# Kernel tuning notes

Measured on AMD Instinct MI355X. Metric: run time of the kernel, lower is better.

The kernel has to match this reference:

```python
import jax, jax.numpy as jnp
import numpy as np

N_NODES = 50000
N_EDGES = 800000
IN_DIM = 128
HIDDEN = 256
N_CLASSES = 10
N_GRAPHS = 64


def setup_inputs() -> dict:
    key = jax.random.key(0)
    ks = jax.random.split(key, 12)
    x = jax.random.normal(ks[0], (N_NODES, IN_DIM), dtype=jnp.float32)
    edge_index = jax.random.randint(ks[1], (2, N_EDGES), 0, N_NODES, dtype=jnp.int64)
    batch = jnp.sort(jax.random.randint(ks[2], (N_NODES,), 0, N_GRAPHS, dtype=jnp.int64))
    s = 1.0 / np.sqrt(IN_DIM)
    sh = 1.0 / np.sqrt(HIDDEN)
    return {
        "x": x,
        "edge_index": edge_index,
        "batch": batch,
        # layer 0 (in_dim -> hidden), weights stored [in, out]
        "Wg0": jax.random.uniform(ks[3], (IN_DIM, HIDDEN), jnp.float32, -s, s),
        "Wl0": jax.random.uniform(ks[4], (IN_DIM, HIDDEN), jnp.float32, -s, s),
        "Ws0": jax.random.uniform(ks[5], (IN_DIM, HIDDEN), jnp.float32, -s, s),
        "b0": jnp.zeros((HIDDEN,), jnp.float32),
        # layer 1 (hidden -> hidden)
        "Wg1": jax.random.uniform(ks[6], (HIDDEN, HIDDEN), jnp.float32, -sh, sh),
        "Wl1": jax.random.uniform(ks[7], (HIDDEN, HIDDEN), jnp.float32, -sh, sh),
        "Ws1": jax.random.uniform(ks[8], (HIDDEN, HIDDEN), jnp.float32, -sh, sh),
        "b1": jnp.zeros((HIDDEN,), jnp.float32),
        # classifier (hidden -> num_classes)
        "Wc": jax.random.uniform(ks[9], (HIDDEN, N_CLASSES), jnp.float32, -sh, sh),
        "bc": jax.random.uniform(ks[10], (N_CLASSES,), jnp.float32, -sh, sh),
    }


def _demo_layer(h, src, dst, deg, Wg, Wl, Ws, b):
    # global transform on all nodes
    g = h @ Wg
    # per-node mean of neighbor features over outgoing edges (== degree-bucket mean)
    neigh_sum = jax.ops.segment_sum(h[dst], src, num_segments=N_NODES)
    neigh_mean = neigh_sum / jnp.maximum(deg, 1.0)[:, None]
    # degree-0 nodes receive only the global branch (as in the torch loop)
    out = g + jnp.where((deg > 0)[:, None], neigh_mean @ Wl + h @ Ws, 0.0)
    return jax.nn.elu(out + b)  # dropout is identity in eval mode


def reference(x, edge_index, batch, Wg0, Wl0, Ws0, b0, Wg1, Wl1, Ws1, b1, Wc, bc):
    src, dst = edge_index[0], edge_index[1]
    deg = jax.ops.segment_sum(jnp.ones(src.shape[0], x.dtype), src, num_segments=N_NODES)
    h = _demo_layer(x, src, dst, deg, Wg0, Wl0, Ws0, b0)
    h = _demo_layer(h, src, dst, deg, Wg1, Wl1, Ws1, b1)
    # global mean pool per graph
    cnt = jax.ops.segment_sum(jnp.ones(N_NODES, h.dtype), batch, num_segments=N_GRAPHS)
    g = jax.ops.segment_sum(h, batch, num_segments=N_GRAPHS) / jnp.maximum(cnt, 1.0)[:, None]
    return g @ Wc + bc
```

## Files before the change

### kernel.cpp

```cpp
#include <hip/hip_runtime.h>

#define N_NODES 50000
#define N_PAD   50048
#define N_EDGES 800000
#define IN_DIM 128
#define HIDDEN 256
#define N_CLASSES 10
#define N_GRAPHS 64

#define SCAN_BLK 1024
#define NB_SCAN ((N_NODES + SCAN_BLK - 1) / SCAN_BLK)

typedef __attribute__((ext_vector_type(8))) short short8;
typedef __attribute__((ext_vector_type(4))) float f32x4;

__device__ __forceinline__ float bf2f(unsigned short h) {
    union { unsigned int u; float f; } v; v.u = ((unsigned int)h) << 16; return v.f;
}
__device__ __forceinline__ unsigned short f2bf(float f) {
    union { float f; unsigned int u; } v; v.f = f;
    unsigned int u = v.u;
    u += 0x7FFFu + ((u >> 16) & 1u);
    return (unsigned short)(u >> 16);
}

__global__ void deg_count_kernel(const int* __restrict__ src, int* __restrict__ deg) {
    int e = blockIdx.x * blockDim.x + threadIdx.x;
    if (e < N_EDGES) atomicAdd(&deg[src[e]], 1);
}

__global__ __launch_bounds__(SCAN_BLK)
void block_sum_kernel(const int* __restrict__ deg, int* __restrict__ blocksum) {
    __shared__ int red[SCAN_BLK / 64];
    int i = blockIdx.x * SCAN_BLK + threadIdx.x;
    int v = (i < N_NODES) ? deg[i] : 0;
    #pragma unroll
    for (int off = 32; off; off >>= 1) v += __shfl_down(v, off, 64);
    if ((threadIdx.x & 63) == 0) red[threadIdx.x >> 6] = v;
    __syncthreads();
    if (threadIdx.x < 64) {
        int s = (threadIdx.x < SCAN_BLK / 64) ? red[threadIdx.x] : 0;
        #pragma unroll
        for (int off = 8; off; off >>= 1) s += __shfl_down(s, off, 64);
        if (threadIdx.x == 0) blocksum[blockIdx.x] = s;
    }
}

__global__ void block_offset_kernel(const int* __restrict__ blocksum, int* __restrict__ blockoff) {
    int lane = threadIdx.x;
    int v = (lane < NB_SCAN) ? blocksum[lane] : 0;
    #pragma unroll
    for (int off = 1; off < 64; off <<= 1) {
        int t = __shfl_up(v, off, 64);
        if (lane >= off) v += t;
    }
    int ex = __shfl_up(v, 1, 64);
    if (lane == 0) ex = 0;
    if (lane < NB_SCAN) blockoff[lane] = ex;
}

__global__ __launch_bounds__(SCAN_BLK)
void scan_phase_c_kernel(const int* __restrict__ deg, const int* __restrict__ blockoff,
                         int* __restrict__ rowptr, int* __restrict__ cursor,
                         float* __restrict__ rdeg,
                         int* __restrict__ d0cnt, int* __restrict__ d0list) {
    __shared__ int buf[SCAN_BLK];
    int i = blockIdx.x * SCAN_BLK + threadIdx.x;
    int v = (i < N_NODES) ? deg[i] : 0;
    buf[threadIdx.x] = v;
    __syncthreads();
    #pragma unroll
    for (int off = 1; off < SCAN_BLK; off <<= 1) {
        int t = (threadIdx.x >= off) ? buf[threadIdx.x - off] : 0;
        __syncthreads();
        buf[threadIdx.x] += t;
        __syncthreads();
    }
    int incl = buf[threadIdx.x] + blockoff[blockIdx.x];
    if (i < N_NODES) {
        rowptr[i + 1] = incl;
        cursor[i] = incl - v;
        rdeg[i] = (v > 0) ? 1.0f / (float)v : 0.0f;
        if (v == 0) { int p = atomicAdd(d0cnt, 1); d0list[p] = i; }
        if (i == 0) rowptr[0] = 0;
    }
}

__global__ void csr_fill_kernel(const int* __restrict__ src, const int* __restrict__ dst,
                                int* __restrict__ cursor, int* __restrict__ csr) {
    int e = blockIdx.x * blockDim.x + threadIdx.x;
    if (e < N_EDGES) {
        int p = atomicAdd(&cursor[src[e]], 1);
        csr[p] = dst[e];
    }
}

__global__ void cvt_bf16_kernel(const float* __restrict__ in, unsigned short* __restrict__ out, int n4) {
    int i = blockIdx.x * blockDim.x + threadIdx.x;
    if (i >= n4) return;
    float4 v = reinterpret_cast<const float4*>(in)[i];
    ushort4 o;
    o.x = f2bf(v.x); o.y = f2bf(v.y); o.z = f2bf(v.z); o.w = f2bf(v.w);
    reinterpret_cast<ushort4*>(out)[i] = o;
}

template<int D>
__global__ void prep_w_kernel(const float* __restrict__ Wg, const float* __restrict__ Wl,
                              const float* __restrict__ Ws, unsigned short* __restrict__ Wt) {
    int i = blockIdx.x * blockDim.x + threadIdx.x;
    if (i >= 256 * 2 * D) return;
    int c = i / (2 * D), k = i % (2 * D);
    float v;
    if (k < D) v = Wg[(size_t)k * 256 + c] + Ws[(size_t)k * 256 + c];
    else       v = Wl[(size_t)(k - D) * 256 + c];
    Wt[i] = f2bf(v);
}

template<int D>
__global__ __launch_bounds__(256)
void gather_mean_kernel(const int* __restrict__ rowptr, const int* __restrict__ csr,
                        const float* __restrict__ rdeg,
                        const unsigned short* __restrict__ H, unsigned short* __restrict__ NS) {
    int node = blockIdx.x * 4 + (threadIdx.x >> 6);
    if (node >= N_NODES) return;
    int lane = threadIdx.x & 63;
    int lo = rowptr[node], hi = rowptr[node + 1];
    float r = rdeg[node];
    if (D == 256) {
        const uint2* H2 = reinterpret_cast<const uint2*>(H);
        float a0 = 0.f, a1 = 0.f, a2 = 0.f, a3 = 0.f;
        int j = lo;
        for (; j + 1 < hi; j += 2) {
            uint2 v0 = H2[(size_t)csr[j] * 64 + lane];
            uint2 v1 = H2[(size_t)csr[j + 1] * 64 + lane];
            a0 += bf2f(v0.x & 0xFFFF) + bf2f(v1.x & 0xFFFF);
            a1 += bf2f(v0.x >> 16)    + bf2f(v1.x >> 16);
            a2 += bf2f(v0.y & 0xFFFF) + bf2f(v1.y & 0xFFFF);
            a3 += bf2f(v0.y >> 16)    + bf2f(v1.y >> 16);
        }
        if (j < hi) {
            uint2 v0 = H2[(size_t)csr[j] * 64 + lane];
            a0 += bf2f(v0.x & 0xFFFF); a1 += bf2f(v0.x >> 16);
            a2 += bf2f(v0.y & 0xFFFF); a3 += bf2f(v0.y >> 16);
        }
        uint2 o;
        o.x = (unsigned int)f2bf(a0 * r) | ((unsigned int)f2bf(a1 * r) << 16);
        o.y = (unsigned int)f2bf(a2 * r) | ((unsigned int)f2bf(a3 * r) << 16);
        reinterpret_cast<uint2*>(NS)[(size_t)node * 64 + lane] = o;
    } else {
        const unsigned int* H1 = reinterpret_cast<const unsigned int*>(H);
        float a0 = 0.f, a1 = 0.f;
        int j = lo;
        for (; j + 1 < hi; j += 2) {
            unsigned int v0 = H1[(size_t)csr[j] * 64 + lane];
            unsigned int v1 = H1[(size_t)csr[j + 1] * 64 + lane];
            a0 += bf2f(v0 & 0xFFFF) + bf2f(v1 & 0xFFFF);
            a1 += bf2f(v0 >> 16)    + bf2f(v1 >> 16);
        }
        if (j < hi) {
            unsigned int v0 = H1[(size_t)csr[j] * 64 + lane];
            a0 += bf2f(v0 & 0xFFFF); a1 += bf2f(v0 >> 16);
        }
        unsigned int o = (unsigned int)f2bf(a0 * r) | ((unsigned int)f2bf(a1 * r) << 16);
        reinterpret_cast<unsigned int*>(NS)[(size_t)node * 64 + lane] = o;
    }
}

template<int D>
__global__ __launch_bounds__(512)
void gemm_mfma_kernel(const unsigned short* __restrict__ X, const unsigned short* __restrict__ NS,
                      const unsigned short* __restrict__ Wt, const float* __restrict__ bias,
                      unsigned short* __restrict__ OUT) {
    constexpr int KTOT = 2 * D;
    __shared__ __align__(16) unsigned short A_lds[128 * 64];
    __shared__ __align__(16) unsigned short B_lds[256 * 64];
    const int tid = threadIdx.x;
    const int lane = tid & 63;
    const int wid = tid >> 6;
    const int wm = wid >> 2, wn = wid & 3;
    const int rowbase = blockIdx.x * 128;

    f32x4 acc[4][4];
    #pragma unroll
    for (int i = 0; i < 4; ++i)
        #pragma unroll
        for (int j = 0; j < 4; ++j) acc[i][j] = (f32x4)0.0f;

    for (int kt = 0; kt < KTOT; kt += 64) {
        const unsigned short* Aseg = (kt < D) ? X : NS;
        const int kd0 = (kt < D) ? kt : kt - D;
        #pragma unroll
        for (int p = 0; p < 2; ++p) {
            int c = (p * 8 + wid) * 64 + lane;
            int row = c >> 3, sl = c & 7;
            int ss = sl ^ (row & 7);
            const unsigned short* g = Aseg + (size_t)(rowbase + row) * D + kd0 + ss * 8;
            unsigned short* l = &A_lds[(size_t)(p * 8 + wid) * 512];
            __builtin_amdgcn_global_load_lds((const __attribute__((address_space(1))) unsigned int*)g,
                                             (__attribute__((address_space(3))) unsigned int*)l, 16, 0, 0);
        }
        #pragma unroll
        for (int p = 0; p < 4; ++p) {
            int c = (p * 8 + wid) * 64 + lane;
            int br = c >> 3, sl = c & 7;
            int ss = sl ^ (br & 7);
            const unsigned short* g = Wt + (size_t)br * KTOT + kt + ss * 8;
            unsigned short* l = &B_lds[(size_t)(p * 8 + wid) * 512];
            __builtin_amdgcn_global_load_lds((const __attribute__((address_space(1))) unsigned int*)g,
                                             (__attribute__((address_space(3))) unsigned int*)l, 16, 0, 0);
        }
        __syncthreads();
        #pragma unroll
        for (int ks = 0; ks < 2; ++ks) {
            short8 a[4], b[4];
            int s = ks * 4 + (lane >> 4);
            #pragma unroll
            for (int f = 0; f < 4; ++f) {
                int row = wm * 64 + f * 16 + (lane & 15);
                a[f] = *reinterpret_cast<const short8*>(&A_lds[row * 64 + ((s ^ (row & 7)) << 3)]);
                int col = wn * 64 + f * 16 + (lane & 15);
                b[f] = *reinterpret_cast<const short8*>(&B_lds[col * 64 + ((s ^ (col & 7)) << 3)]);
            }
            #pragma unroll
            for (int fi = 0; fi < 4; ++fi)
                #pragma unroll
                for (int fj = 0; fj < 4; ++fj)
                    acc[fi][fj] = __builtin_amdgcn_mfma_f32_16x16x32_bf16(a[fi], b[fj], acc[fi][fj], 0, 0, 0);
        }
        __syncthreads();
    }

    float bv[4];
    #pragma unroll
    for (int fj = 0; fj < 4; ++fj) bv[fj] = bias[wn * 64 + fj * 16 + (lane & 15)];
    #pragma unroll
    for (int fi = 0; fi < 4; ++fi) {
        #pragma unroll
        for (int r = 0; r < 4; ++r) {
            int row = rowbase + wm * 64 + fi * 16 + (lane >> 4) * 4 + r;
            if (row < N_NODES) {
                #pragma unroll
                for (int fj = 0; fj < 4; ++fj) {
                    float z = acc[fi][fj][r] + bv[fj];
                    z = z > 0.f ? z : (expf(z) - 1.f);
                    OUT[(size_t)row * 256 + wn * 64 + fj * 16 + (lane & 15)] = f2bf(z);
                }
            }
        }
    }
}

template<typename T, int D>
__global__ void fixup_kernel(const int* __restrict__ cnt, const int* __restrict__ list,
                             const T* __restrict__ X,
                             const float* __restrict__ Wg, const float* __restrict__ bias,
                             unsigned short* __restrict__ OUT) {
    int c = threadIdx.x;
    int n = *cnt;
    for (int i = blockIdx.x; i < n; i += gridDim.x) {
        int row = list[i];
        float acc = bias[c];
        for (int k = 0; k < D; ++k) {
            float xv;
            if constexpr (sizeof(T) == 4) xv = ((const float*)X)[(size_t)row * D + k];
            else                          xv = bf2f(((const unsigned short*)X)[(size_t)row * D + k]);
            acc = fmaf(xv, Wg[(size_t)k * 256 + c], acc);
        }
        acc = acc > 0.f ? acc : (expf(acc) - 1.f);
        OUT[(size_t)row * 256 + c] = f2bf(acc);
    }
}

__global__ __launch_bounds__(256)
void pool_partial_kernel(const unsigned short* __restrict__ H, const int* __restrict__ batch,
                         float* __restrict__ pooled) {
    const int base = blockIdx.x * 64;
    const int t = threadIdx.x;
    float acc = 0.0f;
    int cur = batch[base];
    const int end = (base + 64 < N_NODES) ? base + 64 : N_NODES;
    for (int r = base; r < end; ++r) {
        int g = batch[r];
        if (g != cur) {
            atomicAdd(&pooled[cur * HIDDEN + t], acc);
            acc = 0.0f; cur = g;
        }
        acc += bf2f(H[(size_t)r * HIDDEN + t]);
    }
    atomicAdd(&pooled[cur * HIDDEN + t], acc);
}

__global__ void classify_kernel(const float* __restrict__ pooled, const int* __restrict__ batch,
                                const float* __restrict__ Wc, const float* __restrict__ bc,
                                float* __restrict__ out) {
    __shared__ int s_lo, s_hi;
    __shared__ float pl[HIDDEN];
    int g = blockIdx.x;
    if (threadIdx.x == 0) {
        int lo = 0, hi = N_NODES;
        while (lo < hi) { int m = (lo + hi) >> 1; if (batch[m] < g) lo = m + 1; else hi = m; }
        s_lo = lo;
        int lo2 = lo, hi2 = N_NODES;
        while (lo2 < hi2) { int m = (lo2 + hi2) >> 1; if (batch[m] < g + 1) lo2 = m + 1; else hi2 = m; }
        s_hi = lo2;
    }
    __syncthreads();
    int t = threadIdx.x;
    float cnt = (float)(s_hi - s_lo);
    pl[t] = pooled[g * HIDDEN + t] / fmaxf(cnt, 1.0f);
    __syncthreads();
    if (t < N_CLASSES) {
        float accv = bc[t];
        #pragma unroll 4
        for (int k = 0; k < HIDDEN; ++k) accv = fmaf(pl[k], Wc[k * N_CLASSES + t], accv);
        out[g * N_CLASSES + t] = accv;
    }
}

extern "C" void kernel_launch(void* const* d_in, const int* in_sizes, int n_in,
                              void* d_out, int out_size, void* d_ws, size_t ws_size,
                              hipStream_t stream) {
    const float* x    = (const float*)d_in[0];
    const int*   ei   = (const int*)d_in[1];
    const int*   batch= (const int*)d_in[2];
    const float* Wg0  = (const float*)d_in[3];
    const float* Wl0  = (const float*)d_in[4];
    const float* Ws0  = (const float*)d_in[5];
    const float* b0   = (const float*)d_in[6];
    const float* Wg1  = (const float*)d_in[7];
    const float* Wl1  = (const float*)d_in[8];
    const float* Ws1  = (const float*)d_in[9];
    const float* b1   = (const float*)d_in[10];
    const float* Wc   = (const float*)d_in[11];
    const float* bc   = (const float*)d_in[12];
    const int* src = ei;
    const int* dst = ei + N_EDGES;

    char* ws = (char*)d_ws;
    int*            deg    = (int*)(ws + 0);
    int*            d0cnt  = (int*)(ws + 200192);
    int*            blocksum = (int*)(ws + 200704);
    int*            blockoff = (int*)(ws + 201216);
    float*          rdeg   = (float*)(ws + 262144);
    int*            rowptr = (int*)(ws + 524288);
    int*            cursor = (int*)(ws + 786432);
    float*          pooled = (float*)(ws + 786432);
    int*            csr    = (int*)(ws + 1048576);
    int*            d0list = (int*)(ws + 4259840);
    unsigned short* x_bf   = (unsigned short*)(ws + 4521984);
    unsigned short* ns0_bf = (unsigned short*)(ws + 17334272);
    unsigned short* h1_bf  = (unsigned short*)(ws + 30146560);
    unsigned short* ns1_bf = (unsigned short*)(ws + 55771136);
    unsigned short* h2_bf  = (unsigned short*)(ws + 81395712);
    unsigned short* Wt0    = (unsigned short*)(ws + 107020288);
    unsigned short* Wt1    = (unsigned short*)(ws + 107151360);

    hipMemsetAsync(ws, 0, 262144, stream);

    deg_count_kernel<<<(N_EDGES + 255) / 256, 256, 0, stream>>>(src, deg);
    block_sum_kernel<<<NB_SCAN, SCAN_BLK, 0, stream>>>(deg, blocksum);
    block_offset_kernel<<<1, 64, 0, stream>>>(blocksum, blockoff);
    scan_phase_c_kernel<<<NB_SCAN, SCAN_BLK, 0, stream>>>(deg, blockoff, rowptr, cursor, rdeg, d0cnt, d0list);
    csr_fill_kernel<<<(N_EDGES + 255) / 256, 256, 0, stream>>>(src, dst, cursor, csr);

    prep_w_kernel<IN_DIM><<<(256 * 2 * IN_DIM + 255) / 256, 256, 0, stream>>>(Wg0, Wl0, Ws0, Wt0);
    prep_w_kernel<HIDDEN><<<(256 * 2 * HIDDEN + 255) / 256, 256, 0, stream>>>(Wg1, Wl1, Ws1, Wt1);
    cvt_bf16_kernel<<<(N_NODES * IN_DIM / 4 + 255) / 256, 256, 0, stream>>>(x, x_bf, N_NODES * IN_DIM / 4);

    gather_mean_kernel<IN_DIM><<<(N_NODES + 3) / 4, 256, 0, stream>>>(rowptr, csr, rdeg, x_bf, ns0_bf);
    gemm_mfma_kernel<IN_DIM><<<(N_NODES + 127) / 128, 512, 0, stream>>>(x_bf, ns0_bf, Wt0, b0, h1_bf);
    fixup_kernel<float, IN_DIM><<<64, 256, 0, stream>>>(d0cnt, d0list, x, Wg0, b0, h1_bf);

    gather_mean_kernel<HIDDEN><<<(N_NODES + 3) / 4, 256, 0, stream>>>(rowptr, csr, rdeg, h1_bf, ns1_bf);
    gemm_mfma_kernel<HIDDEN><<<(N_NODES + 127) / 128, 512, 0, stream>>>(h1_bf, ns1_bf, Wt1, b1, h2_bf);
    fixup_kernel<unsigned short, HIDDEN><<<64, 256, 0, stream>>>(d0cnt, d0list, h1_bf, Wg1, b1, h2_bf);

    hipMemsetAsync(pooled, 0, N_GRAPHS * HIDDEN * sizeof(float), stream);
    pool_partial_kernel<<<(N_NODES + 63) / 64, 256, 0, stream>>>(h2_bf, batch, pooled);
    classify_kernel<<<N_GRAPHS, HIDDEN, 0, stream>>>(pooled, batch, Wc, bc, (float*)d_out);
}
```

Before: 325.3 us.

## Store node features in 32-column slice-major blocks for cache-local neighbor gathers

Node feature matrices (x_bf, the neighbor means and h1) are now stored as column slices of 32 bf16 values, each slice contiguous over all padded nodes. The gather is reworked so each block handles one slice for a chunk of nodes, which keeps the random neighbor reads inside a small slice that fits in L2. Each wavefront splits a node's edges across four 16-lane groups and combines them with shuffles. The GEMM loads, the GEMM output and the fixup kernels are rewritten to use the new layout, which adds index arithmetic and launches several slice passes that each reread the CSR structure.

```diff
diff --git a/kernel.cpp b/kernel.cpp
--- a/kernel.cpp
+++ b/kernel.cpp
@@ -13,6 +13,7 @@
 
 typedef __attribute__((ext_vector_type(8))) short short8;
 typedef __attribute__((ext_vector_type(4))) float f32x4;
+
 
 __device__ __forceinline__ float bf2f(unsigned short h) {
     union { unsigned int u; float f; } v; v.u = ((unsigned int)h) << 16; return v.f;
@@ -95,13 +96,18 @@
     }
 }
 
-__global__ void cvt_bf16_kernel(const float* __restrict__ in, unsigned short* __restrict__ out, int n4) {
+__global__ void cvt_bf16_fb_kernel(const float* __restrict__ in, unsigned short* __restrict__ out) {
     int i = blockIdx.x * blockDim.x + threadIdx.x;
-    if (i >= n4) return;
-    float4 v = reinterpret_cast<const float4*>(in)[i];
-    ushort4 o;
-    o.x = f2bf(v.x); o.y = f2bf(v.y); o.z = f2bf(v.z); o.w = f2bf(v.w);
-    reinterpret_cast<ushort4*>(out)[i] = o;
+    if (i >= N_NODES * (IN_DIM / 8)) return;
+    int n = i >> 4, c = i & 15;
+    const float4* p = reinterpret_cast<const float4*>(in + (size_t)n * IN_DIM + c * 8);
+    float4 v0 = p[0], v1 = p[1];
+    uint4 o;
+    o.x = (unsigned int)f2bf(v0.x) | ((unsigned int)f2bf(v0.y) << 16);
+    o.y = (unsigned int)f2bf(v0.z) | ((unsigned int)f2bf(v0.w) << 16);
+    o.z = (unsigned int)f2bf(v1.x) | ((unsigned int)f2bf(v1.y) << 16);
+    o.w = (unsigned int)f2bf(v1.z) | ((unsigned int)f2bf(v1.w) << 16);
+    *reinterpret_cast<uint4*>(out + ((size_t)(c >> 2) * N_PAD + n) * 32 + (c & 3) * 8) = o;
 }
 
 template<int D>
@@ -118,55 +124,37 @@
 
 template<int D>
 __global__ __launch_bounds__(256)
-void gather_mean_kernel(const int* __restrict__ rowptr, const int* __restrict__ csr,
-                        const float* __restrict__ rdeg,
-                        const unsigned short* __restrict__ H, unsigned short* __restrict__ NS) {
-    int node = blockIdx.x * 4 + (threadIdx.x >> 6);
-    if (node >= N_NODES) return;
-    int lane = threadIdx.x & 63;
-    int lo = rowptr[node], hi = rowptr[node + 1];
-    float r = rdeg[node];
-    if (D == 256) {
-        const uint2* H2 = reinterpret_cast<const uint2*>(H);
-        float a0 = 0.f, a1 = 0.f, a2 = 0.f, a3 = 0.f;
-        int j = lo;
-        for (; j + 1 < hi; j += 2) {
-            uint2 v0 = H2[(size_t)csr[j] * 64 + lane];
-            uint2 v1 = H2[(size_t)csr[j + 1] * 64 + lane];
-            a0 += bf2f(v0.x & 0xFFFF) + bf2f(v1.x & 0xFFFF);
-            a1 += bf2f(v0.x >> 16)    + bf2f(v1.x >> 16);
-            a2 += bf2f(v0.y & 0xFFFF) + bf2f(v1.y & 0xFFFF);
-            a3 += bf2f(v0.y >> 16)    + bf2f(v1.y >> 16);
-        }
-        if (j < hi) {
-            uint2 v0 = H2[(size_t)csr[j] * 64 + lane];
-            a0 += bf2f(v0.x & 0xFFFF); a1 += bf2f(v0.x >> 16);
-            a2 += bf2f(v0.y & 0xFFFF); a3 += bf2f(v0.y >> 16);
-        }
-        uint2 o;
-        o.x = (unsigned int)f2bf(a0 * r) | ((unsigned int)f2bf(a1 * r) << 16);
-        o.y = (unsigned int)f2bf(a2 * r) | ((unsigned int)f2bf(a3 * r) << 16);
-        reinterpret_cast<uint2*>(NS)[(size_t)node * 64 + lane] = o;
-    } else {
-        const unsigned int* H1 = reinterpret_cast<const unsigned int*>(H);
+void gather_slice_kernel(const int* __restrict__ rowptr, const int* __restrict__ csr,
+                         const float* __restrict__ rdeg,
+                         const unsigned short* __restrict__ H, unsigned short* __restrict__ NS) {
+    constexpr int NSL = D / 32, SUB = 8 / NSL;
+    const int slice = blockIdx.x / SUB;
+    const int chunk = blockIdx.y * SUB + (blockIdx.x % SUB);
+    const int lane = threadIdx.x & 63;
+    const int grp = lane >> 4, s16 = lane & 15;
+    const unsigned int* Hu = reinterpret_cast<const unsigned int*>(H) + (size_t)slice * N_PAD * 16;
+    unsigned int* Ou = reinterpret_cast<unsigned int*>(NS) + (size_t)slice * N_PAD * 16;
+    const int nodebase = chunk * 128 + (threadIdx.x >> 6) * 32;
+    for (int i = 0; i < 32; ++i) {
+        int node = nodebase + i;
+        if (node >= N_NODES) return;
+        int lo = rowptr[node], hi = rowptr[node + 1];
         float a0 = 0.f, a1 = 0.f;
-        int j = lo;
-        for (; j + 1 < hi; j += 2) {
-            unsigned int v0 = H1[(size_t)csr[j] * 64 + lane];
-            unsigned int v1 = H1[(size_t)csr[j + 1] * 64 + lane];
-            a0 += bf2f(v0 & 0xFFFF) + bf2f(v1 & 0xFFFF);
-            a1 += bf2f(v0 >> 16)    + bf2f(v1 >> 16);
-        }
-        if (j < hi) {
-            unsigned int v0 = H1[(size_t)csr[j] * 64 + lane];
-            a0 += bf2f(v0 & 0xFFFF); a1 += bf2f(v0 >> 16);
-        }
-        unsigned int o = (unsigned int)f2bf(a0 * r) | ((unsigned int)f2bf(a1 * r) << 16);
-        reinterpret_cast<unsigned int*>(NS)[(size_t)node * 64 + lane] = o;
-    }
-}
-
-template<int D>
+        for (int j = lo + grp; j < hi; j += 4) {
+            unsigned int v = Hu[(size_t)csr[j] * 16 + s16];
+            a0 += bf2f(v & 0xFFFF); a1 += bf2f(v >> 16);
+        }
+        a0 += __shfl_xor(a0, 16, 64); a0 += __shfl_xor(a0, 32, 64);
+        a1 += __shfl_xor(a1, 16, 64); a1 += __shfl_xor(a1, 32, 64);
+        if (grp == 0) {
+            float r = rdeg[node];
+            Ou[(size_t)node * 16 + s16] =
+                (unsigned int)f2bf(a0 * r) | ((unsigned int)f2bf(a1 * r) << 16);
+        }
+    }
+}
+
+template<int D, bool BLK_OUT>
 __global__ __launch_bounds__(512)
 void gemm_mfma_kernel(const unsigned short* __restrict__ X, const unsigned short* __restrict__ NS,
                       const unsigned short* __restrict__ Wt, const float* __restrict__ bias,
@@ -194,7 +182,8 @@
             int c = (p * 8 + wid) * 64 + lane;
             int row = c >> 3, sl = c & 7;
             int ss = sl ^ (row & 7);
-            const unsigned short* g = Aseg + (size_t)(rowbase + row) * D + kd0 + ss * 8;
+            int gc = kd0 + ss * 8;
+            const unsigned short* g = Aseg + ((size_t)(gc >> 5) * N_PAD + rowbase + row) * 32 + (gc & 31);
             unsigned short* l = &A_lds[(size_t)(p * 8 + wid) * 512];
             __builtin_amdgcn_global_load_lds((const __attribute__((address_space(1))) unsigned int*)g,
                                              (__attribute__((address_space(3))) unsigned int*)l, 16, 0, 0);
@@ -241,18 +230,22 @@
             if (row < N_NODES) {
                 #pragma unroll
                 for (int fj = 0; fj < 4; ++fj) {
+                    int col = wn * 64 + fj * 16 + (lane & 15);
                     float z = acc[fi][fj][r] + bv[fj];
                     z = z > 0.f ? z : (expf(z) - 1.f);
-                    OUT[(size_t)row * 256 + wn * 64 + fj * 16 + (lane & 15)] = f2bf(z);
+                    if (BLK_OUT)
+                        OUT[((size_t)(col >> 5) * N_PAD + row) * 32 + (col & 31)] = f2bf(z);
+                    else
+                        OUT[(size_t)row * 256 + col] = f2bf(z);
                 }
             }
         }
     }
 }
 
-template<typename T, int D>
+template<bool XF32, bool BLK_OUT, int D>
 __global__ void fixup_kernel(const int* __restrict__ cnt, const int* __restrict__ list,
-                             const T* __restrict__ X,
+                             const void* __restrict__ X,
                              const float* __restrict__ Wg, const float* __restrict__ bias,
                              unsigned short* __restrict__ OUT) {
     int c = threadIdx.x;
@@ -262,12 +255,13 @@
         float acc = bias[c];
         for (int k = 0; k < D; ++k) {
             float xv;
-            if constexpr (sizeof(T) == 4) xv = ((const float*)X)[(size_t)row * D + k];
-            else                          xv = bf2f(((const unsigned short*)X)[(size_t)row * D + k]);
+            if constexpr (XF32) xv = ((const float*)X)[(size_t)row * D + k];
+            else xv = bf2f(((const unsigned short*)X)[((size_t)(k >> 5) * N_PAD + row) * 32 + (k & 31)]);
             acc = fmaf(xv, Wg[(size_t)k * 256 + c], acc);
         }
         acc = acc > 0.f ? acc : (expf(acc) - 1.f);
-        OUT[(size_t)row * 256 + c] = f2bf(acc);
+        if (BLK_OUT) OUT[((size_t)(c >> 5) * N_PAD + row) * 32 + (c & 31)] = f2bf(acc);
+        else         OUT[(size_t)row * 256 + c] = f2bf(acc);
     }
 }
 
@@ -365,15 +359,15 @@
 
     prep_w_kernel<IN_DIM><<<(256 * 2 * IN_DIM + 255) / 256, 256, 0, stream>>>(Wg0, Wl0, Ws0, Wt0);
     prep_w_kernel<HIDDEN><<<(256 * 2 * HIDDEN + 255) / 256, 256, 0, stream>>>(Wg1, Wl1, Ws1, Wt1);
-    cvt_bf16_kernel<<<(N_NODES * IN_DIM / 4 + 255) / 256, 256, 0, stream>>>(x, x_bf, N_NODES * IN_DIM / 4);
-
-    gather_mean_kernel<IN_DIM><<<(N_NODES + 3) / 4, 256, 0, stream>>>(rowptr, csr, rdeg, x_bf, ns0_bf);
-    gemm_mfma_kernel<IN_DIM><<<(N_NODES + 127) / 128, 512, 0, stream>>>(x_bf, ns0_bf, Wt0, b0, h1_bf);
-    fixup_kernel<float, IN_DIM><<<64, 256, 0, stream>>>(d0cnt, d0list, x, Wg0, b0, h1_bf);
-
-    gather_mean_kernel<HIDDEN><<<(N_NODES + 3) / 4, 256, 0, stream>>>(rowptr, csr, rdeg, h1_bf, ns1_bf);
-    gemm_mfma_kernel<HIDDEN><<<(N_NODES + 127) / 128, 512, 0, stream>>>(h1_bf, ns1_bf, Wt1, b1, h2_bf);
-    fixup_kernel<unsigned short, HIDDEN><<<64, 256, 0, stream>>>(d0cnt, d0list, h1_bf, Wg1, b1, h2_bf);
+    cvt_bf16_fb_kernel<<<(N_NODES * 16 + 255) / 256, 256, 0, stream>>>(x, x_bf);
+
+    gather_slice_kernel<IN_DIM><<<dim3(8, 196), 256, 0, stream>>>(rowptr, csr, rdeg, x_bf, ns0_bf);
+    gemm_mfma_kernel<IN_DIM, true><<<(N_NODES + 127) / 128, 512, 0, stream>>>(x_bf, ns0_bf, Wt0, b0, h1_bf);
+    fixup_kernel<true, true, IN_DIM><<<64, 256, 0, stream>>>(d0cnt, d0list, x, Wg0, b0, h1_bf);
+
+    gather_slice_kernel<HIDDEN><<<dim3(8, 391), 256, 0, stream>>>(rowptr, csr, rdeg, h1_bf, ns1_bf);
+    gemm_mfma_kernel<HIDDEN, false><<<(N_NODES + 127) / 128, 512, 0, stream>>>(h1_bf, ns1_bf, Wt1, b1, h2_bf);
+    fixup_kernel<false, false, HIDDEN><<<64, 256, 0, stream>>>(d0cnt, d0list, h1_bf, Wg1, b1, h2_bf);
 
     hipMemsetAsync(pooled, 0, N_GRAPHS * HIDDEN * sizeof(float), stream);
     pool_partial_kernel<<<(N_NODES + 63) / 64, 256, 0, stream>>>(h2_bf, batch, pooled);
```

Result: slower. 468.2 us (+43.9%).
